# Kernel tuning notes

Measured on AMD Instinct MI355X. Metric: run time of the kernel, lower is better.

The kernel has to match this reference:

```python
import jax, jax.numpy as jnp
import numpy as np

B = 2048          # batch_size
D = 512           # embedding dim
TEMP = 0.1        # temperature
EPS = 1e-8        # torch CosineSimilarity eps


def _neg_idx(batch_size):
    n = 2 * batch_size
    mask = np.eye(n) + np.eye(n, n, k=-batch_size) + np.eye(n, n, k=batch_size)
    mask = (1 - mask).astype(bool)           # True at negatives
    # each row has exactly n-2 True entries -> fixed-shape gather indices
    return np.nonzero(mask)[1].reshape(n, n - 2)

_NEG_IDX = jnp.asarray(_neg_idx(B))           # [2B, 2B-2]
_ROWS = jnp.arange(2 * B)[:, None]            # [2B, 1]


def _cos_sim_matrix(r):
    # r: [2B, D] -> [2B, 2B] cosine similarity
    norm = jnp.maximum(jnp.linalg.norm(r, axis=-1, keepdims=True), EPS)
    rn = r / norm
    return rn @ rn.T


def _pos(sim):
    # diag(sim, +B) and diag(sim, -B), concatenated -> [2B, 1]
    l = jnp.diagonal(sim, offset=B)
    r = jnp.diagonal(sim, offset=-B)
    return jnp.concatenate([l, r])[:, None]


def _neg(sim):
    # masked gather of off-(diag,+B,-B) entries -> [2B, 2B-2]
    return sim[_ROWS, _NEG_IDX]


def _ce_sum_label0(logits):
    # CrossEntropyLoss(reduction='sum') with all labels == 0
    return -jnp.sum(jax.nn.log_softmax(logits, axis=-1)[:, 0])


def setup_inputs() -> dict:
    key = jax.random.key(0)
    k1, k2, k3, k4 = jax.random.split(key, 4)
    return {
        "z_ori": jax.random.normal(k1, (B, D), jnp.float32),
        "z_hard_pos": jax.random.normal(k2, (B, D), jnp.float32),
        "z_soft_pos": jax.random.normal(k3, (B, D), jnp.float32),
        "z_soft_neg": jax.random.normal(k4, (B, D), jnp.float32),
    }


def reference(z_ori, z_hard_pos, z_soft_pos, z_soft_neg):
    sim_ori_hp = _cos_sim_matrix(jnp.concatenate([z_ori, z_hard_pos], axis=0))
    sim_ori_sp = _cos_sim_matrix(jnp.concatenate([z_ori, z_soft_pos], axis=0))
    sim_ori_sn = _cos_sim_matrix(jnp.concatenate([z_ori, z_soft_neg], axis=0))
    sim_hp_sp = _cos_sim_matrix(jnp.concatenate([z_hard_pos, z_soft_pos], axis=0))
    sim_hp_sn = _cos_sim_matrix(jnp.concatenate([z_hard_pos, z_soft_neg], axis=0))
    sim_sp_sn = _cos_sim_matrix(jnp.concatenate([z_soft_pos, z_soft_neg], axis=0))

    pos_ori_sn = _pos(sim_ori_sn)
    pos_hp_sn = _pos(sim_hp_sn)
    pos_sp_sn = _pos(sim_sp_sn)

    pos_ori_hp = _pos(sim_ori_hp)
    neg_ori_hp = _neg(sim_ori_hp)
    pos_ori_sp = _pos(sim_ori_sp)
    neg_ori_sp = _neg(sim_ori_sp)
    pos_hp_sp = _pos(sim_hp_sp)
    neg_hp_sp = _neg(sim_hp_sp)

    logits_ori_hp = jnp.concatenate([pos_ori_hp, neg_ori_hp, pos_ori_sn], axis=1) / TEMP
    logits_ori_sp = jnp.concatenate([pos_ori_sp, neg_ori_sp, pos_ori_sn], axis=1) / TEMP
    logits_hp_sp = jnp.concatenate([pos_hp_sp, neg_hp_sp, pos_hp_sn, pos_sp_sn], axis=1) / TEMP

    denom = 2.0 * B
    return (
        _ce_sum_label0(logits_ori_hp) / denom,
        _ce_sum_label0(logits_ori_sp) / denom,
        _ce_sum_label0(logits_hp_sp) / denom,
    )
```

## Files before the change

### kernel.cpp

```cpp
#include <hip/hip_runtime.h>
#include <hip/hip_bf16.h>

#define Bn 2048
#define Dn 512

typedef float f32x4 __attribute__((ext_vector_type(4)));
typedef long long ll2 __attribute__((ext_vector_type(2)));

typedef __attribute__((address_space(1))) const unsigned int gas_u32;
typedef __attribute__((address_space(3))) unsigned int las_u32;

__device__ __forceinline__ void gload16(const void* g, void* l) {
  __builtin_amdgcn_global_load_lds((gas_u32*)g, (las_u32*)l, 16, 0, 0);
}

__global__ __launch_bounds__(256) void normalize_kernel(
    const float* __restrict__ in0, const float* __restrict__ in1,
    const float* __restrict__ in2, const float* __restrict__ in3,
    unsigned char* __restrict__ nm8, float* __restrict__ rs, float* __restrict__ dd) {
  __shared__ float sv[4][Dn];
  __shared__ float red[4][6];
  int row = blockIdx.x;
  int wave = threadIdx.x >> 6, lane = threadIdx.x & 63;

  int g0 = blockIdx.x * 256 + threadIdx.x;
  if (g0 < 9 * Bn) rs[g0] = 0.0f;

  const float* src =
      (wave == 0 ? in0 : wave == 1 ? in1 : wave == 2 ? in2 : in3) + (size_t)row * Dn;
  int k = lane * 8;
  float4 x0 = *(const float4*)(src + k);
  float4 x1 = *(const float4*)(src + k + 4);
  float v[8] = {x0.x, x0.y, x0.z, x0.w, x1.x, x1.y, x1.z, x1.w};
  float ss = 0.f;
#pragma unroll
  for (int e = 0; e < 8; e++) ss = fmaf(v[e], v[e], ss);
#pragma unroll
  for (int off = 1; off < 64; off <<= 1) ss += __shfl_xor(ss, off, 64);
  float scale = 1.0f / fmaxf(sqrtf(ss), 1e-8f);
  float nv[8];
#pragma unroll
  for (int e = 0; e < 8; e++) {
    nv[e] = v[e] * scale;
    sv[wave][k + e] = nv[e];
  }
  if (wave < 3) {
    unsigned int lo = __builtin_amdgcn_cvt_pk_fp8_f32(nv[0], nv[1], 0u, false);
    lo = __builtin_amdgcn_cvt_pk_fp8_f32(nv[2], nv[3], lo, true);
    unsigned int hi = __builtin_amdgcn_cvt_pk_fp8_f32(nv[4], nv[5], 0u, false);
    hi = __builtin_amdgcn_cvt_pk_fp8_f32(nv[6], nv[7], hi, true);
    uint2 pk; pk.x = lo; pk.y = hi;
    int kb = lane >> 3, g = lane & 7;
    int p = ((g & 3) << 1) | (g >> 2);
    *(uint2*)(nm8 + ((size_t)wave * Bn + row) * Dn + kb * 64 + p * 8) = pk;
  }
  __syncthreads();

  int t = threadIdx.x;
  float o0 = sv[0][2 * t], o1 = sv[0][2 * t + 1];
  float h0 = sv[1][2 * t], h1 = sv[1][2 * t + 1];
  float p0 = sv[2][2 * t], p1 = sv[2][2 * t + 1];
  float n0 = sv[3][2 * t], n1 = sv[3][2 * t + 1];
  float s[6];
  s[0] = fmaf(o0, h0, o1 * h1);
  s[1] = fmaf(o0, p0, o1 * p1);
  s[2] = fmaf(h0, p0, h1 * p1);
  s[3] = fmaf(o0, n0, o1 * n1);
  s[4] = fmaf(h0, n0, h1 * n1);
  s[5] = fmaf(p0, n0, p1 * n1);
#pragma unroll
  for (int off = 1; off < 64; off <<= 1) {
#pragma unroll
    for (int j = 0; j < 6; j++) s[j] += __shfl_xor(s[j], off, 64);
  }
  if (lane == 0) {
#pragma unroll
    for (int j = 0; j < 6; j++) red[wave][j] = s[j];
  }
  __syncthreads();
  if (threadIdx.x < 6) {
    int j = threadIdx.x;
    dd[j * Bn + row] = red[0][j] + red[1][j] + red[2][j] + red[3][j];
  }
}

#define GBM 128
#define GBK 64
#define NKT 8
#define NBUF 4

__global__ __launch_bounds__(512) void gemm_fp8_kernel(const unsigned char* __restrict__ nm8,
                                                       float* __restrict__ rs) {
  __shared__ unsigned char lds[NBUF * 16384];

  int id = ((int)blockIdx.x & 7) * 147 + ((int)blockIdx.x >> 3);
  int by = 0, rem = id, cnt = 48;
  while (rem >= cnt) { rem -= cnt; by++; cnt--; }
  int bx = by + rem;
  int u = by >> 4, v = bx >> 4;
  int rrow, rcol;
  if (u == v) { rrow = u; rcol = u; }
  else if (u == 0) { if (v == 1) { rrow = 3; rcol = 4; } else { rrow = 5; rcol = 6; } }
  else { rrow = 7; rcol = 8; }

  const unsigned char* gA = nm8 + ((size_t)u * Bn + (size_t)(by & 15) * GBM) * Dn;
  const unsigned char* gB = nm8 + ((size_t)v * Bn + (size_t)(bx & 15) * GBM) * Dn;

  int tid = threadIdx.x, lane = tid & 63, wave = tid >> 6;
  int wr = wave >> 2, wc = wave & 3;
  int c = lane & 15, rgrp = lane >> 4;
  int ru = ((rgrp ^ ((c >> 1) & 3)) << 4);

  int srow = tid >> 2;
  int suu = (tid & 3) ^ ((srow >> 1) & 3);
  size_t aoff = (size_t)srow * Dn + suu * 16;
  const unsigned char* sA = gA + aoff;
  const unsigned char* sB = gB + aoff;
  int dbase = wave << 10;

#define STAGE(kt, j)                                         \
  {                                                          \
    unsigned char* d = lds + (j) * 16384;                    \
    gload16(sA + (kt) * GBK, d + dbase);                     \
    gload16(sB + (kt) * GBK, d + 8192 + dbase);              \
  }

  f32x4 acc[4][2] = {};

  STAGE(0, 0);
  STAGE(1, 1);
  STAGE(2, 2);
  asm volatile("s_waitcnt vmcnt(4)" ::: "memory");
  __builtin_amdgcn_s_barrier();
  asm volatile("" ::: "memory");

#pragma unroll
  for (int t = 0; t < NKT; ++t) {
    const unsigned char* As = lds + (t & 3) * 16384;
    const unsigned char* Bs = As + 8192;
    if (t + 3 < NKT) STAGE(t + 3, (t + 3) & 3);
    ll2 a[4];
    ll2 b[2];
#pragma unroll
    for (int mi = 0; mi < 4; ++mi)
      a[mi] = *(const ll2*)(As + (wr * 64 + mi * 16 + c) * 64 + ru);
#pragma unroll
    for (int ni = 0; ni < 2; ++ni)
      b[ni] = *(const ll2*)(Bs + (wc * 32 + ni * 16 + c) * 64 + ru);
    __builtin_amdgcn_s_setprio(1);
#pragma unroll
    for (int ks = 0; ks < 2; ++ks)
#pragma unroll
      for (int mi = 0; mi < 4; ++mi)
#pragma unroll
        for (int ni = 0; ni < 2; ++ni)
          acc[mi][ni] =
              __builtin_amdgcn_mfma_f32_16x16x32_fp8_fp8(a[mi][ks], b[ni][ks], acc[mi][ni], 0, 0, 0);
    __builtin_amdgcn_s_setprio(0);
    if (t + 3 < NKT) {
      asm volatile("s_waitcnt vmcnt(4)" ::: "memory");
    } else if (t + 2 < NKT) {
      asm volatile("s_waitcnt vmcnt(2)" ::: "memory");
    } else if (t + 1 < NKT) {
      asm volatile("s_waitcnt vmcnt(0)" ::: "memory");
    }
    __builtin_amdgcn_s_barrier();
    asm volatile("" ::: "memory");
    __builtin_amdgcn_sched_barrier(0);
  }
#undef STAGE

  float* crow = (float*)lds;
  float* ccol = crow + GBM;
  __syncthreads();
  if (tid < 2 * GBM) ((float*)lds)[tid] = 0.0f;
  __syncthreads();

  bool skip_diag = (by == bx);
#pragma unroll
  for (int mi = 0; mi < 4; ++mi)
#pragma unroll
    for (int ni = 0; ni < 2; ++ni)
#pragma unroll
      for (int r = 0; r < 4; ++r) {
        int lrow = wr * 64 + mi * 16 + rgrp * 4 + r;
        int lcol = wc * 32 + ni * 16 + c;
        float e = __expf(10.0f * acc[mi][ni][r] - 10.0f);
        acc[mi][ni][r] = (skip_diag && lrow == lcol) ? 0.0f : e;
      }

#pragma unroll
  for (int mi = 0; mi < 4; ++mi)
#pragma unroll
    for (int r = 0; r < 4; ++r) {
      float val = acc[mi][0][r] + acc[mi][1][r];
      val += __shfl_xor(val, 1, 64);
      val += __shfl_xor(val, 2, 64);
      val += __shfl_xor(val, 4, 64);
      val += __shfl_xor(val, 8, 64);
      if (c == 0) atomicAdd(&crow[wr * 64 + mi * 16 + rgrp * 4 + r], val);
    }
#pragma unroll
  for (int ni = 0; ni < 2; ++ni) {
    float cv = 0.f;
#pragma unroll
    for (int mi = 0; mi < 4; ++mi)
#pragma unroll
      for (int r = 0; r < 4; ++r) cv += acc[mi][ni][r];
    cv += __shfl_xor(cv, 16, 64);
    cv += __shfl_xor(cv, 32, 64);
    if (lane < 16) atomicAdd(&ccol[wc * 32 + ni * 16 + c], cv);
  }
  __syncthreads();

  float* rs_row = rs + rrow * Bn + (by & 15) * GBM;
  if (tid < GBM) {
    atomicAdd(rs_row + tid, crow[tid]);
  } else if (tid < 2 * GBM && by != bx) {
    float* rs_col = rs + rcol * Bn + (bx & 15) * GBM;
    atomicAdd(rs_col + (tid - GBM), ccol[tid - GBM]);
  }
}

__global__ __launch_bounds__(1024) void final_kernel(const float* __restrict__ rs,
                                                     const float* __restrict__ dd,
                                                     float* __restrict__ out) {
  int tid = threadIdx.x;
  float l1 = 0.f, l2 = 0.f, l3 = 0.f;
  for (int i = tid; i < Bn; i += 1024) {
    float doh = dd[i], dop = dd[Bn + i], dhp = dd[2 * Bn + i];
    float ea = __expf(10.0f * dd[3 * Bn + i] - 10.0f);
    float eb = __expf(10.0f * dd[4 * Bn + i] - 10.0f);
    float ec = __expf(10.0f * dd[5 * Bn + i] - 10.0f);
    float r0 = rs[i], r1 = rs[Bn + i], r2 = rs[2 * Bn + i];
    float r3 = rs[3 * Bn + i], r4 = rs[4 * Bn + i], r5 = rs[5 * Bn + i];
    float r6 = rs[6 * Bn + i], r7 = rs[7 * Bn + i], r8 = rs[8 * Bn + i];
    l1 += 20.0f + logf(r0 + r3 + ea) + logf(r4 + r1 + ea) - 20.0f * doh;
    l2 += 20.0f + logf(r0 + r5 + ea) + logf(r6 + r2 + ea) - 20.0f * dop;
    l3 += 20.0f + logf(r1 + r7 + eb + ec) + logf(r8 + r2 + eb + ec) - 20.0f * dhp;
  }
  __shared__ float red[3][1024];
  red[0][tid] = l1; red[1][tid] = l2; red[2][tid] = l3;
  __syncthreads();
  for (int s = 512; s > 0; s >>= 1) {
    if (tid < s) {
      red[0][tid] += red[0][tid + s];
      red[1][tid] += red[1][tid + s];
      red[2][tid] += red[2][tid + s];
    }
    __syncthreads();
  }
  if (tid == 0) {
    out[0] = red[0][0] / 4096.0f;
    out[1] = red[1][0] / 4096.0f;
    out[2] = red[2][0] / 4096.0f;
  }
}

extern "C" void kernel_launch(void* const* d_in, const int* in_sizes, int n_in,
                              void* d_out, int out_size, void* d_ws, size_t ws_size,
                              hipStream_t stream) {
  const float* z0 = (const float*)d_in[0];
  const float* z1 = (const float*)d_in[1];
  const float* z2 = (const float*)d_in[2];
  const float* z3 = (const float*)d_in[3];
  float* out = (float*)d_out;

  unsigned char* nm8 = (unsigned char*)d_ws;
  float* rs = (float*)((char*)d_ws + (size_t)3 * Bn * Dn);
  float* dd = rs + 9 * Bn;

  hipLaunchKernelGGL(normalize_kernel, dim3(2048), dim3(256), 0, stream,
                     z0, z1, z2, z3, nm8, rs, dd);
  hipLaunchKernelGGL(gemm_fp8_kernel, dim3(1176), dim3(512), 0, stream, nm8, rs);
  hipLaunchKernelGGL(final_kernel, dim3(1), dim3(1024), 0, stream, rs, dd, out);
}
```

Measured before the change: 44.83 us.

## Load fp8 GEMM operands directly from global into registers, dropping LDS staging

The GEMM kernel no longer stages A/B tiles through LDS with global_load_lds and a 4-deep buffer ring. Each wave now loads its MFMA fragments straight from global memory into a 3-slot register ring, prefetching two k-steps ahead. This removes the LDS round trip and the per-iteration barriers and frees most shared memory, which may allow higher occupancy. The cost is redundant global and L2 traffic, because waves sharing rows reload the same data, and small 16-byte strided loads that coalesce less well.

```diff
diff --git a/kernel.cpp b/kernel.cpp
--- a/kernel.cpp
+++ b/kernel.cpp
@@ -6,13 +6,6 @@
 
 typedef float f32x4 __attribute__((ext_vector_type(4)));
 typedef long long ll2 __attribute__((ext_vector_type(2)));
-
-typedef __attribute__((address_space(1))) const unsigned int gas_u32;
-typedef __attribute__((address_space(3))) unsigned int las_u32;
-
-__device__ __forceinline__ void gload16(const void* g, void* l) {
-  __builtin_amdgcn_global_load_lds((gas_u32*)g, (las_u32*)l, 16, 0, 0);
-}
 
 __global__ __launch_bounds__(256) void normalize_kernel(
     const float* __restrict__ in0, const float* __restrict__ in1,
@@ -85,14 +78,10 @@
 }
 
 #define GBM 128
-#define GBK 64
 #define NKT 8
-#define NBUF 4
 
 __global__ __launch_bounds__(512) void gemm_fp8_kernel(const unsigned char* __restrict__ nm8,
                                                        float* __restrict__ rs) {
-  __shared__ unsigned char lds[NBUF * 16384];
-
   int id = ((int)blockIdx.x & 7) * 147 + ((int)blockIdx.x >> 3);
   int by = 0, rem = id, cnt = 48;
   while (rem >= cnt) { rem -= cnt; by++; cnt--; }
@@ -109,71 +98,53 @@
   int tid = threadIdx.x, lane = tid & 63, wave = tid >> 6;
   int wr = wave >> 2, wc = wave & 3;
   int c = lane & 15, rgrp = lane >> 4;
-  int ru = ((rgrp ^ ((c >> 1) & 3)) << 4);
-
-  int srow = tid >> 2;
-  int suu = (tid & 3) ^ ((srow >> 1) & 3);
-  size_t aoff = (size_t)srow * Dn + suu * 16;
-  const unsigned char* sA = gA + aoff;
-  const unsigned char* sB = gB + aoff;
-  int dbase = wave << 10;
-
-#define STAGE(kt, j)                                         \
-  {                                                          \
-    unsigned char* d = lds + (j) * 16384;                    \
-    gload16(sA + (kt) * GBK, d + dbase);                     \
-    gload16(sB + (kt) * GBK, d + 8192 + dbase);              \
-  }
+
+  const unsigned char* pa[4];
+  const unsigned char* pb[2];
+#pragma unroll
+  for (int mi = 0; mi < 4; ++mi)
+    pa[mi] = gA + (size_t)(wr * 64 + mi * 16 + c) * Dn + rgrp * 16;
+#pragma unroll
+  for (int ni = 0; ni < 2; ++ni)
+    pb[ni] = gB + (size_t)(wc * 32 + ni * 16 + c) * Dn + rgrp * 16;
 
   f32x4 acc[4][2] = {};
-
-  STAGE(0, 0);
-  STAGE(1, 1);
-  STAGE(2, 2);
-  asm volatile("s_waitcnt vmcnt(4)" ::: "memory");
-  __builtin_amdgcn_s_barrier();
-  asm volatile("" ::: "memory");
+  ll2 ar[3][4], br[3][2];
+
+#pragma unroll
+  for (int mi = 0; mi < 4; ++mi) {
+    ar[0][mi] = *(const ll2*)(pa[mi]);
+    ar[1][mi] = *(const ll2*)(pa[mi] + 64);
+  }
+#pragma unroll
+  for (int ni = 0; ni < 2; ++ni) {
+    br[0][ni] = *(const ll2*)(pb[ni]);
+    br[1][ni] = *(const ll2*)(pb[ni] + 64);
+  }
 
 #pragma unroll
   for (int t = 0; t < NKT; ++t) {
-    const unsigned char* As = lds + (t & 3) * 16384;
-    const unsigned char* Bs = As + 8192;
-    if (t + 3 < NKT) STAGE(t + 3, (t + 3) & 3);
-    ll2 a[4];
-    ll2 b[2];
-#pragma unroll
-    for (int mi = 0; mi < 4; ++mi)
-      a[mi] = *(const ll2*)(As + (wr * 64 + mi * 16 + c) * 64 + ru);
-#pragma unroll
-    for (int ni = 0; ni < 2; ++ni)
-      b[ni] = *(const ll2*)(Bs + (wc * 32 + ni * 16 + c) * 64 + ru);
-    __builtin_amdgcn_s_setprio(1);
+    const int cs = t % 3, ns = (t + 2) % 3;
+    if (t + 2 < NKT) {
+#pragma unroll
+      for (int mi = 0; mi < 4; ++mi) ar[ns][mi] = *(const ll2*)(pa[mi] + (t + 2) * 64);
+#pragma unroll
+      for (int ni = 0; ni < 2; ++ni) br[ns][ni] = *(const ll2*)(pb[ni] + (t + 2) * 64);
+    }
 #pragma unroll
     for (int ks = 0; ks < 2; ++ks)
 #pragma unroll
       for (int mi = 0; mi < 4; ++mi)
 #pragma unroll
         for (int ni = 0; ni < 2; ++ni)
-          acc[mi][ni] =
-              __builtin_amdgcn_mfma_f32_16x16x32_fp8_fp8(a[mi][ks], b[ni][ks], acc[mi][ni], 0, 0, 0);
-    __builtin_amdgcn_s_setprio(0);
-    if (t + 3 < NKT) {
-      asm volatile("s_waitcnt vmcnt(4)" ::: "memory");
-    } else if (t + 2 < NKT) {
-      asm volatile("s_waitcnt vmcnt(2)" ::: "memory");
-    } else if (t + 1 < NKT) {
-      asm volatile("s_waitcnt vmcnt(0)" ::: "memory");
-    }
-    __builtin_amdgcn_s_barrier();
-    asm volatile("" ::: "memory");
-    __builtin_amdgcn_sched_barrier(0);
-  }
-#undef STAGE
-
-  float* crow = (float*)lds;
-  float* ccol = crow + GBM;
-  __syncthreads();
-  if (tid < 2 * GBM) ((float*)lds)[tid] = 0.0f;
+          acc[mi][ni] = __builtin_amdgcn_mfma_f32_16x16x32_fp8_fp8(ar[cs][mi][ks], br[cs][ni][ks],
+                                                                   acc[mi][ni], 0, 0, 0);
+  }
+
+  __shared__ float cb[2 * GBM];
+  float* crow = cb;
+  float* ccol = cb + GBM;
+  if (tid < 2 * GBM) cb[tid] = 0.0f;
   __syncthreads();
 
   bool skip_diag = (by == bx);
```

After: 83.09 us. +85.4%, slower.

## Cut GEMM LDS buffers to three for occupancy and parallelize final reduction

Applied to the files above, without the earlier changes.

The fp8 GEMM pipeline drops from four LDS stages to three (48KB instead of 64KB) and prefetches two tiles ahead instead of three, with a launch-bounds hint asking for more resident waves per CU. The final loss kernel now runs as 8 blocks of 256 threads, each handling one element per thread and atomically adding its partial sums into the output, which the normalize kernel zeroes first. The aim is more concurrent GEMM workgroups per CU and a shorter serial tail in the last kernel. In exchange, the shallower prefetch can expose more load latency, and the output is now summed with float atomics.

```diff
diff --git a/kernel.cpp b/kernel.cpp
--- a/kernel.cpp
+++ b/kernel.cpp
@@ -17,7 +17,8 @@
 __global__ __launch_bounds__(256) void normalize_kernel(
     const float* __restrict__ in0, const float* __restrict__ in1,
     const float* __restrict__ in2, const float* __restrict__ in3,
-    unsigned char* __restrict__ nm8, float* __restrict__ rs, float* __restrict__ dd) {
+    unsigned char* __restrict__ nm8, float* __restrict__ rs, float* __restrict__ dd,
+    float* __restrict__ out) {
   __shared__ float sv[4][Dn];
   __shared__ float red[4][6];
   int row = blockIdx.x;
@@ -25,6 +26,7 @@
 
   int g0 = blockIdx.x * 256 + threadIdx.x;
   if (g0 < 9 * Bn) rs[g0] = 0.0f;
+  if (g0 < 3) out[g0] = 0.0f;
 
   const float* src =
       (wave == 0 ? in0 : wave == 1 ? in1 : wave == 2 ? in2 : in3) + (size_t)row * Dn;
@@ -87,10 +89,10 @@
 #define GBM 128
 #define GBK 64
 #define NKT 8
-#define NBUF 4
-
-__global__ __launch_bounds__(512) void gemm_fp8_kernel(const unsigned char* __restrict__ nm8,
-                                                       float* __restrict__ rs) {
+#define NBUF 3
+
+__global__ __launch_bounds__(512, 6) void gemm_fp8_kernel(const unsigned char* __restrict__ nm8,
+                                                          float* __restrict__ rs) {
   __shared__ unsigned char lds[NBUF * 16384];
 
   int id = ((int)blockIdx.x & 7) * 147 + ((int)blockIdx.x >> 3);
@@ -129,16 +131,15 @@
 
   STAGE(0, 0);
   STAGE(1, 1);
-  STAGE(2, 2);
-  asm volatile("s_waitcnt vmcnt(4)" ::: "memory");
+  asm volatile("s_waitcnt vmcnt(2)" ::: "memory");
   __builtin_amdgcn_s_barrier();
   asm volatile("" ::: "memory");
 
 #pragma unroll
   for (int t = 0; t < NKT; ++t) {
-    const unsigned char* As = lds + (t & 3) * 16384;
+    const unsigned char* As = lds + (t % 3) * 16384;
     const unsigned char* Bs = As + 8192;
-    if (t + 3 < NKT) STAGE(t + 3, (t + 3) & 3);
+    if (t + 2 < NKT) STAGE(t + 2, (t + 2) % 3);
     ll2 a[4];
     ll2 b[2];
 #pragma unroll
@@ -154,12 +155,10 @@
       for (int mi = 0; mi < 4; ++mi)
 #pragma unroll
         for (int ni = 0; ni < 2; ++ni)
-          acc[mi][ni] =
-              __builtin_amdgcn_mfma_f32_16x16x32_fp8_fp8(a[mi][ks], b[ni][ks], acc[mi][ni], 0, 0, 0);
+          acc[mi][ni] = __builtin_amdgcn_mfma_f32_16x16x32_fp8_fp8(
+              a[mi][ks], b[ni][ks], acc[mi][ni], 0, 0, 0);
     __builtin_amdgcn_s_setprio(0);
-    if (t + 3 < NKT) {
-      asm volatile("s_waitcnt vmcnt(4)" ::: "memory");
-    } else if (t + 2 < NKT) {
+    if (t + 2 < NKT) {
       asm volatile("s_waitcnt vmcnt(2)" ::: "memory");
     } else if (t + 1 < NKT) {
       asm volatile("s_waitcnt vmcnt(0)" ::: "memory");
@@ -222,27 +221,26 @@
   }
 }
 
-__global__ __launch_bounds__(1024) void final_kernel(const float* __restrict__ rs,
-                                                     const float* __restrict__ dd,
-                                                     float* __restrict__ out) {
+__global__ __launch_bounds__(256) void final_kernel(const float* __restrict__ rs,
+                                                    const float* __restrict__ dd,
+                                                    float* __restrict__ out) {
+  int i = blockIdx.x * 256 + threadIdx.x;
+  float doh = dd[i], dop = dd[Bn + i], dhp = dd[2 * Bn + i];
+  float ea = __expf(10.0f * dd[3 * Bn + i] - 10.0f);
+  float eb = __expf(10.0f * dd[4 * Bn + i] - 10.0f);
+  float ec = __expf(10.0f * dd[5 * Bn + i] - 10.0f);
+  float r0 = rs[i], r1 = rs[Bn + i], r2 = rs[2 * Bn + i];
+  float r3 = rs[3 * Bn + i], r4 = rs[4 * Bn + i], r5 = rs[5 * Bn + i];
+  float r6 = rs[6 * Bn + i], r7 = rs[7 * Bn + i], r8 = rs[8 * Bn + i];
+  float l1 = 20.0f + logf(r0 + r3 + ea) + logf(r4 + r1 + ea) - 20.0f * doh;
+  float l2 = 20.0f + logf(r0 + r5 + ea) + logf(r6 + r2 + ea) - 20.0f * dop;
+  float l3 = 20.0f + logf(r1 + r7 + eb + ec) + logf(r8 + r2 + eb + ec) - 20.0f * dhp;
+
+  __shared__ float red[3][256];
   int tid = threadIdx.x;
-  float l1 = 0.f, l2 = 0.f, l3 = 0.f;
-  for (int i = tid; i < Bn; i += 1024) {
-    float doh = dd[i], dop = dd[Bn + i], dhp = dd[2 * Bn + i];
-    float ea = __expf(10.0f * dd[3 * Bn + i] - 10.0f);
-    float eb = __expf(10.0f * dd[4 * Bn + i] - 10.0f);
-    float ec = __expf(10.0f * dd[5 * Bn + i] - 10.0f);
-    float r0 = rs[i], r1 = rs[Bn + i], r2 = rs[2 * Bn + i];
-    float r3 = rs[3 * Bn + i], r4 = rs[4 * Bn + i], r5 = rs[5 * Bn + i];
-    float r6 = rs[6 * Bn + i], r7 = rs[7 * Bn + i], r8 = rs[8 * Bn + i];
-    l1 += 20.0f + logf(r0 + r3 + ea) + logf(r4 + r1 + ea) - 20.0f * doh;
-    l2 += 20.0f + logf(r0 + r5 + ea) + logf(r6 + r2 + ea) - 20.0f * dop;
-    l3 += 20.0f + logf(r1 + r7 + eb + ec) + logf(r8 + r2 + eb + ec) - 20.0f * dhp;
-  }
-  __shared__ float red[3][1024];
   red[0][tid] = l1; red[1][tid] = l2; red[2][tid] = l3;
   __syncthreads();
-  for (int s = 512; s > 0; s >>= 1) {
+  for (int s = 128; s > 0; s >>= 1) {
     if (tid < s) {
       red[0][tid] += red[0][tid + s];
       red[1][tid] += red[1][tid + s];
@@ -250,11 +248,7 @@
     }
     __syncthreads();
   }
-  if (tid == 0) {
-    out[0] = red[0][0] / 4096.0f;
-    out[1] = red[1][0] / 4096.0f;
-    out[2] = red[2][0] / 4096.0f;
-  }
+  if (tid < 3) atomicAdd(&out[tid], red[tid][0] * (1.0f / 4096.0f));
 }
 
 extern "C" void kernel_launch(void* const* d_in, const int* in_sizes, int n_in,
@@ -271,7 +265,7 @@
   float* dd = rs + 9 * Bn;
 
   hipLaunchKernelGGL(normalize_kernel, dim3(2048), dim3(256), 0, stream,
-                     z0, z1, z2, z3, nm8, rs, dd);
+                     z0, z1, z2, z3, nm8, rs, dd, out);
   hipLaunchKernelGGL(gemm_fp8_kernel, dim3(1176), dim3(512), 0, stream, nm8, rs);
-  hipLaunchKernelGGL(final_kernel, dim3(1), dim3(1024), 0, stream, rs, dd, out);
-}
+  hipLaunchKernelGGL(final_kernel, dim3(8), dim3(256), 0, stream, rs, dd, out);
+}
```

Measured after the change: 39.94 us, median of 3. 10.9% less time.
